# Performance work log

Hardware: AMD Instinct MI355X
Metric: run time of the kernel (lower is better)

The kernel has to match this reference:

```python
import jax, jax.numpy as jnp
import numpy as np

D_MODEL = 2048
N_HEADS = 16
DH = D_MODEL // N_HEADS
B, S, S_CACHE = 2, 1024, 1024


def setup_inputs() -> dict:
    key = jax.random.key(0)
    ks = jax.random.split(key, 5)
    x = jax.random.normal(ks[0], (B, S, D_MODEL), dtype=jnp.float32)
    k_cache = jax.random.normal(ks[1], (B, N_HEADS, S_CACHE, DH), dtype=jnp.float32)
    v_cache = jax.random.normal(ks[2], (B, N_HEADS, S_CACHE, DH), dtype=jnp.float32)
    qkv = 0.01 * jax.random.normal(ks[3], (3 * D_MODEL, D_MODEL), dtype=jnp.float32)
    wo = 0.01 * jax.random.normal(ks[4], (D_MODEL, D_MODEL), dtype=jnp.float32)
    return {"x": x, "k_cache": k_cache, "v_cache": v_cache,
            "qkv": qkv, "wo": wo, "past_length": S_CACHE}


def reference(x, k_cache, v_cache, qkv, wo, past_length):
    Bn, Sn, D = x.shape
    H, dh = N_HEADS, D // N_HEADS
    # Fused QKV projection: (B,S,3D)
    QKV = jnp.einsum('bsd,ed->bse', x, qkv)
    Q, K, V = jnp.split(QKV, 3, axis=-1)
    # (B,H,S,dh)
    q = Q.reshape(Bn, Sn, H, dh).transpose(0, 2, 1, 3)
    k = K.reshape(Bn, Sn, H, dh).transpose(0, 2, 1, 3)
    v = V.reshape(Bn, Sn, H, dh).transpose(0, 2, 1, 3)
    # KV-cache concat along sequence dim
    k_full = jnp.concatenate([k_cache, k], axis=2)
    v_full = jnp.concatenate([v_cache, v], axis=2)
    S_full = k_full.shape[2]
    # Causal mask shifted by past_length: query i attends to keys j <= i + past_length
    rows = jnp.arange(Sn)[:, None]
    cols = jnp.arange(S_full)[None, :]
    allowed = cols <= rows + past_length  # (S, S_full)
    scale = 1.0 / jnp.sqrt(jnp.asarray(dh, x.dtype))
    scores = jnp.einsum('bhqd,bhkd->bhqk', q, k_full) * scale
    scores = jnp.where(allowed[None, None], scores, jnp.finfo(scores.dtype).min)
    attn = jax.nn.softmax(scores, axis=-1)
    ctx = jnp.einsum('bhqk,bhkd->bhqd', attn, v_full)
    out = ctx.transpose(0, 2, 1, 3).reshape(Bn, Sn, D)
    out = jnp.einsum('bsd,ed->bse', out, wo)
    return out, k_full, v_full
```

## Files before the change

### kernel.cpp

```cpp
#include <hip/hip_runtime.h>
#include <cstdint>

#define HB 2
#define HS 1024
#define HSF 2048
#define HH 16
#define HDH 128
#define HD 2048
#define HD3 6144
#define HM 2048

typedef __attribute__((ext_vector_type(8))) short bf16x8;
typedef __attribute__((ext_vector_type(4))) float f32x4;
typedef __attribute__((ext_vector_type(16))) float f32x16;
typedef unsigned short u16;
typedef unsigned int u32;

__device__ __forceinline__ u16 f2b(float f) {
    union { float f; u32 u; } v; v.f = f;
    u32 u = v.u;
    return (u16)((u + 0x7FFFu + ((u >> 16) & 1u)) >> 16);
}
__device__ __forceinline__ float b2f(u16 h) {
    union { u32 u; float f; } v; v.u = ((u32)h) << 16; return v.f;
}

__device__ __forceinline__ f32x4 mfma16x16(bf16x8 a, bf16x8 b, f32x4 c) {
    return __builtin_amdgcn_mfma_f32_16x16x32_bf16(a, b, c, 0, 0, 0);
}
__device__ __forceinline__ f32x16 mfma32x32(bf16x8 a, bf16x8 b, f32x16 c) {
    return __builtin_amdgcn_mfma_f32_32x32x16_bf16(a, b, c, 0, 0, 0);
}
__device__ __forceinline__ void pl32swap(u32 &a, u32 &b) {
    asm volatile("v_permlane32_swap_b32 %0, %1" : "+v"(a), "+v"(b));
}

#define GLD16(gp, lp) __builtin_amdgcn_global_load_lds( \
    (__attribute__((address_space(1))) void*)(gp), \
    (__attribute__((address_space(3))) void*)(lp), 16, 0, 0)

__global__ __launch_bounds__(256) void k_prep(
    const float* __restrict__ x,  u16* __restrict__ xb,  int n0,
    const float* __restrict__ qkv, u16* __restrict__ qkvb, int n1,
    const float* __restrict__ wo,  u16* __restrict__ wob, int n2,
    const float* __restrict__ kc, const float* __restrict__ vc,
    float* __restrict__ kf, float* __restrict__ vf,
    u16* __restrict__ kb, u16* __restrict__ vt)
{
    const int bid = blockIdx.x;
    const int tid = threadIdx.x;
    if (bid < 512) {
        __shared__ u16 Lt[128 * 66];
        int bh = bid >> 4, st = (bid & 15) << 6;
        size_t cbase = (size_t)bh * (HS * HDH) + (size_t)st * HDH;
        size_t fbase = (size_t)bh * (HSF * HDH) + (size_t)st * HDH;
        #pragma unroll
        for (int i = 0; i < 8; ++i) {
            int ci = i * 256 + tid;
            float4 kv = ((const float4*)(kc + cbase))[ci];
            ((float4*)(kf + fbase))[ci] = kv;
            ushort4 k4;
            k4.x = f2b(kv.x); k4.y = f2b(kv.y); k4.z = f2b(kv.z); k4.w = f2b(kv.w);
            ((ushort4*)(kb + fbase))[ci] = k4;
        }
        #pragma unroll
        for (int i = 0; i < 8; ++i) {
            int ci = i * 256 + tid;
            int r = ci >> 5, c = ci & 31;
            float4 vv = ((const float4*)(vc + cbase))[ci];
            ((float4*)(vf + fbase))[ci] = vv;
            int dh = c * 4;
            Lt[(dh + 0) * 66 + r] = f2b(vv.x);
            Lt[(dh + 1) * 66 + r] = f2b(vv.y);
            Lt[(dh + 2) * 66 + r] = f2b(vv.z);
            Lt[(dh + 3) * 66 + r] = f2b(vv.w);
        }
        __syncthreads();
        u16* vtb = vt + (size_t)bh * (HDH * HSF) + st;
        #pragma unroll
        for (int i = 0; i < 4; ++i) {
            int ci = i * 256 + tid;
            int dh = ci >> 3, cs = (ci & 7) * 8;
            const u16* lr = &Lt[dh * 66 + cs];
            ushort4 lo, hi2;
            lo.x = lr[0]; lo.y = lr[1]; lo.z = lr[2]; lo.w = lr[3];
            hi2.x = lr[4]; hi2.y = lr[5]; hi2.z = lr[6]; hi2.w = lr[7];
            u16* dst = vtb + (size_t)dh * HSF + cs;
            *(ushort4*)dst = lo;
            *(ushort4*)(dst + 4) = hi2;
        }
    } else {
        int i = (bid - 512) * 256 + tid;
        const int st_ = ((int)gridDim.x - 512) * 256;
        const int nt = n0 + n1 + n2;
        for (; i < nt; i += st_) {
            const float* s; u16* d; int j = i;
            if (j < n0) { s = x; d = xb; }
            else if (j < n0 + n1) { j -= n0; s = qkv; d = qkvb; }
            else { j -= n0 + n1; s = wo; d = wob; }
            float4 v = ((const float4*)s)[j];
            ushort4 o;
            o.x = f2b(v.x); o.y = f2b(v.y); o.z = f2b(v.z); o.w = f2b(v.w);
            ((ushort4*)d)[j] = o;
        }
    }
}

__global__ __launch_bounds__(256, 2) void k_gemm_qkv(
    const u16* __restrict__ A, const u16* __restrict__ Bw, int K,
    u16* __restrict__ qb, float* __restrict__ kf, float* __restrict__ vf,
    u16* __restrict__ kb, u16* __restrict__ vt)
{
    __shared__ __align__(16) u16 As[2 * 128 * 32];
    __shared__ __align__(16) u16 Bs[2 * 128 * 32];
    const int tid = threadIdx.x;
    const int w = tid >> 6, lane = tid & 63;
    const int wm = w >> 1, wn = w & 1;
    const int lcol = lane & 15, lhi = lane >> 4;

    const int nb = (int)gridDim.x, per = nb >> 3;
    const int bf = (int)blockIdx.x;
    const int t = (bf & 7) * per + (bf >> 3);
    const int m0 = (t & 15) * 128, n0 = (t >> 4) * 128;

    const int srow = lane >> 2;
    const int scol = ((lane & 3) ^ ((lane >> 4) & 2)) * 8;
    const int c0 = w * 2, c1 = w * 2 + 1;
    const u16* Ag0 = A + (size_t)(m0 + c0 * 16 + srow) * K + scol;
    const u16* Ag1 = A + (size_t)(m0 + c1 * 16 + srow) * K + scol;
    const u16* Bg0 = Bw + (size_t)(n0 + c0 * 16 + srow) * K + scol;
    const u16* Bg1 = Bw + (size_t)(n0 + c1 * 16 + srow) * K + scol;

    const int lx = lhi ^ ((lcol >> 2) & 2);

    f32x4 acc[4][4] = {};

    GLD16(Ag0, &As[c0 * 512]);
    GLD16(Ag1, &As[c1 * 512]);
    GLD16(Bg0, &Bs[c0 * 512]);
    GLD16(Bg1, &Bs[c1 * 512]);
    __syncthreads();

    int cur = 0;
    for (int k0 = 0; k0 < K; k0 += 32) {
        if (k0 + 32 < K) {
            int nb_ = (cur ^ 1) * 4096;
            GLD16(Ag0 + k0 + 32, &As[nb_ + c0 * 512]);
            GLD16(Ag1 + k0 + 32, &As[nb_ + c1 * 512]);
            GLD16(Bg0 + k0 + 32, &Bs[nb_ + c0 * 512]);
            GLD16(Bg1 + k0 + 32, &Bs[nb_ + c1 * 512]);
        }
        const int cb = cur * 4096;
        bf16x8 af[4], bfr[4];
        #pragma unroll
        for (int i = 0; i < 4; ++i)
            af[i] = *(const bf16x8*)&As[cb + (wm * 64 + i * 16 + lcol) * 32 + lx * 8];
        #pragma unroll
        for (int i = 0; i < 4; ++i)
            bfr[i] = *(const bf16x8*)&Bs[cb + (wn * 64 + i * 16 + lcol) * 32 + lx * 8];
        __builtin_amdgcn_s_setprio(1);
        #pragma unroll
        for (int i = 0; i < 4; ++i)
            #pragma unroll
            for (int j = 0; j < 4; ++j)
                acc[i][j] = mfma16x16(af[i], bfr[j], acc[i][j]);
        __builtin_amdgcn_s_setprio(0);
        __syncthreads();
        cur ^= 1;
    }

    #pragma unroll
    for (int i = 0; i < 4; ++i) {
      #pragma unroll
      for (int j = 0; j < 4; ++j) {
        #pragma unroll
        for (int r = 0; r < 4; ++r) {
            int m = m0 + wm * 64 + i * 16 + lhi * 4 + r;
            int n = n0 + wn * 64 + j * 16 + lcol;
            float v = acc[i][j][r];
            int b = m >> 10, s = m & 1023;
            int sec = n >> 11, e = n & 2047;
            int h = e >> 7, dh = e & 127;
            int bh = b * HH + h;
            if (sec == 0) {
                qb[((size_t)bh * HS + s) * HDH + dh] = f2b(v * 0.12751742f);
            } else if (sec == 1) {
                size_t idx = ((size_t)bh * HSF + HS + s) * HDH + dh;
                kf[idx] = v; kb[idx] = f2b(v);
            } else {
                size_t idx = ((size_t)bh * HSF + HS + s) * HDH + dh;
                vf[idx] = v;
                vt[((size_t)bh * HDH + dh) * HSF + HS + s] = f2b(v);
            }
        }
      }
    }
}

__global__ __launch_bounds__(256, 4) void k_gemm_out(
    const u16* __restrict__ A, const u16* __restrict__ Bw, int K,
    float* __restrict__ outf)
{
    __shared__ __align__(16) u16 As[2 * 128 * 32];
    __shared__ __align__(16) u16 Bs[2 * 64 * 32];
    const int tid = threadIdx.x;
    const int w = tid >> 6, lane = tid & 63;
    const int wm = w >> 1, wn = w & 1;
    const int lcol = lane & 15, lhi = lane >> 4;

    const int nb = (int)gridDim.x, per = nb >> 3;
    const int bf = (int)blockIdx.x;
    const int t = (bf & 7) * per + (bf >> 3);
    const int m0 = (t & 15) * 128, n0 = (t >> 4) * 64;

    const int srow = lane >> 2;
    const int scol = ((lane & 3) ^ ((lane >> 4) & 2)) * 8;
    const int c0 = w * 2, c1 = w * 2 + 1;
    const u16* Ag0 = A + (size_t)(m0 + c0 * 16 + srow) * K + scol;
    const u16* Ag1 = A + (size_t)(m0 + c1 * 16 + srow) * K + scol;
    const u16* Bg0 = Bw + (size_t)(n0 + w * 16 + srow) * K + scol;

    const int lx = lhi ^ ((lcol >> 2) & 2);

    f32x4 acc[4][2] = {};

    GLD16(Ag0, &As[c0 * 512]);
    GLD16(Ag1, &As[c1 * 512]);
    GLD16(Bg0, &Bs[w * 512]);
    __syncthreads();

    int cur = 0;
    for (int k0 = 0; k0 < K; k0 += 32) {
        if (k0 + 32 < K) {
            GLD16(Ag0 + k0 + 32, &As[(cur ^ 1) * 4096 + c0 * 512]);
            GLD16(Ag1 + k0 + 32, &As[(cur ^ 1) * 4096 + c1 * 512]);
            GLD16(Bg0 + k0 + 32, &Bs[(cur ^ 1) * 2048 + w * 512]);
        }
        const int ca = cur * 4096, cb2 = cur * 2048;
        bf16x8 af[4], bfr[2];
        #pragma unroll
        for (int i = 0; i < 4; ++i)
            af[i] = *(const bf16x8*)&As[ca + (wm * 64 + i * 16 + lcol) * 32 + lx * 8];
        #pragma unroll
        for (int j = 0; j < 2; ++j)
            bfr[j] = *(const bf16x8*)&Bs[cb2 + (wn * 32 + j * 16 + lcol) * 32 + lx * 8];
        __builtin_amdgcn_s_setprio(1);
        #pragma unroll
        for (int i = 0; i < 4; ++i)
            #pragma unroll
            for (int j = 0; j < 2; ++j)
                acc[i][j] = mfma16x16(af[i], bfr[j], acc[i][j]);
        __builtin_amdgcn_s_setprio(0);
        __syncthreads();
        cur ^= 1;
    }

    #pragma unroll
    for (int i = 0; i < 4; ++i)
      #pragma unroll
      for (int j = 0; j < 2; ++j)
        #pragma unroll
        for (int r = 0; r < 4; ++r) {
            int m = m0 + wm * 64 + i * 16 + lhi * 4 + r;
            int n = n0 + wn * 32 + j * 16 + lcol;
            outf[(size_t)m * HD + n] = acc[i][j][r];
        }
}

__global__ __launch_bounds__(256, 3) void k_attn(
    const u16* __restrict__ qb, const u16* __restrict__ kb,
    const u16* __restrict__ vt, u16* __restrict__ pO,
    float* __restrict__ pM, float* __restrict__ pL,
    const int* __restrict__ plp)
{
    __shared__ __align__(16) u16 Ks[64 * 128];
    __shared__ __align__(16) u16 Vs[128 * 64];

    const int past = *plp;
    const int tid = threadIdx.x, w = tid >> 6, lane = tid & 63;
    const int l31 = lane & 31, hi = lane >> 5;

    const int bid = blockIdx.x;
    const int orig = (bid & 7) * 96 + (bid >> 3);
    const int split = orig % 3;
    const int rest = orig / 3;
    const int qblk = rest & 7;
    const int bh = rest >> 3;
    const int q0b = qblk * 128;
    const int q0 = q0b + w * 32;
    const int q = q0 + l31;

    const u16* qx = qb + (size_t)bh * HS * HDH;
    const u16* kx = kb + (size_t)bh * HSF * HDH;
    const u16* vx = vt + (size_t)bh * HDH * HSF;

    bf16x8 qf[8];
    #pragma unroll
    for (int c = 0; c < 8; ++c)
        qf[c] = *(const bf16x8*)&qx[(size_t)q * HDH + c * 16 + hi * 8];

    const int krow0 = w * 16 + (lane >> 4);
    const int kchunk = lane & 15;
    const int vrow0 = w * 32 + (lane >> 3);
    const int vchunk = lane & 7;

    f32x16 o[4] = {};
    float mr = -3e38f, lr = 0.f;

    int nkt = (q0b + 128 + past + 63) >> 6;
    if (nkt > HSF / 64) nkt = HSF / 64;
    const int t0 = (split * nkt) / 3;
    const int t1 = ((split + 1) * nkt) / 3;

    for (int kt = t0; kt < t1; ++kt) {
        const int j0 = kt * 64;
        __syncthreads();
        #pragma unroll
        for (int i = 0; i < 4; ++i) {
            int rk = krow0 + 4 * i;
            GLD16(kx + (size_t)(j0 + rk) * HDH + ((kchunk ^ (rk & 7)) * 8),
                  Ks + w * 2048 + i * 512);
            int rv = vrow0 + 8 * i;
            GLD16(vx + (size_t)rv * HSF + j0 + ((vchunk ^ (rv & 7)) * 8),
                  Vs + w * 2048 + i * 512);
        }
        __syncthreads();

        if (j0 > q0 + 31 + past) continue;

        const char* ksb = (const char*)Ks;
        f32x16 sf0 = {}, sf1 = {};
        const int sw = l31 & 7;
        __builtin_amdgcn_s_setprio(1);
        #pragma unroll
        for (int c = 0; c < 8; ++c) {
            int ch = ((c * 2 + hi) ^ sw) * 16;
            bf16x8 ak0 = *(const bf16x8*)(ksb + l31 * 256 + ch);
            sf0 = mfma32x32(ak0, qf[c], sf0);
            bf16x8 ak1 = *(const bf16x8*)(ksb + (32 + l31) * 256 + ch);
            sf1 = mfma32x32(ak1, qf[c], sf1);
        }
        __builtin_amdgcn_s_setprio(0);

        if (j0 + 63 > q0 + past) {
            #pragma unroll
            for (int r = 0; r < 16; ++r) {
                int ko = (r & 3) + 8 * (r >> 2) + 4 * hi;
                if (j0 + ko > q + past)      sf0[r] = -3e38f;
                if (j0 + 32 + ko > q + past) sf1[r] = -3e38f;
            }
        }
        float pmax = -3e38f;
        #pragma unroll
        for (int r = 0; r < 16; ++r)
            pmax = fmaxf(pmax, fmaxf(sf0[r], sf1[r]));
        pmax = fmaxf(pmax, __shfl_xor(pmax, 32, 64));
        if (!__all((int)(pmax <= mr + 8.f))) {
            float mnew = fmaxf(mr, pmax);
            float alpha = exp2f(mr - mnew);
            mr = mnew;
            lr *= alpha;
            #pragma unroll
            for (int dt = 0; dt < 4; ++dt) o[dt] *= alpha;
        }
        float ps = 0.f;
        #pragma unroll
        for (int r = 0; r < 16; ++r) {
            sf0[r] = exp2f(sf0[r] - mr);
            sf1[r] = exp2f(sf1[r] - mr);
            ps += sf0[r] + sf1[r];
        }
        ps += __shfl_xor(ps, 32, 64);
        lr += ps;

        u32 wA[8], wB[8];
        #pragma unroll
        for (int g = 0; g < 4; ++g) {
            asm("v_cvt_pk_bf16_f32 %0, %1, %2" : "=v"(wA[2*g])   : "v"(sf0[4*g+0]), "v"(sf0[4*g+1]));
            asm("v_cvt_pk_bf16_f32 %0, %1, %2" : "=v"(wA[2*g+1]) : "v"(sf0[4*g+2]), "v"(sf0[4*g+3]));
            asm("v_cvt_pk_bf16_f32 %0, %1, %2" : "=v"(wB[2*g])   : "v"(sf1[4*g+0]), "v"(sf1[4*g+1]));
            asm("v_cvt_pk_bf16_f32 %0, %1, %2" : "=v"(wB[2*g+1]) : "v"(sf1[4*g+2]), "v"(sf1[4*g+3]));
        }
        pl32swap(wA[0], wA[2]); pl32swap(wA[1], wA[3]);
        pl32swap(wA[4], wA[6]); pl32swap(wA[5], wA[7]);
        pl32swap(wB[0], wB[2]); pl32swap(wB[1], wB[3]);
        pl32swap(wB[4], wB[6]); pl32swap(wB[5], wB[7]);
        union uf { u32 u[4]; bf16x8 v; };
        uf pf0, pf1, pf2, pf3;
        pf0.u[0]=wA[0]; pf0.u[1]=wA[1]; pf0.u[2]=wA[2]; pf0.u[3]=wA[3];
        pf1.u[0]=wA[4]; pf1.u[1]=wA[5]; pf1.u[2]=wA[6]; pf1.u[3]=wA[7];
        pf2.u[0]=wB[0]; pf2.u[1]=wB[1]; pf2.u[2]=wB[2]; pf2.u[3]=wB[3];
        pf3.u[0]=wB[4]; pf3.u[1]=wB[5]; pf3.u[2]=wB[6]; pf3.u[3]=wB[7];

        const char* vsb = (const char*)Vs;
        __builtin_amdgcn_s_setprio(1);
        #pragma unroll
        for (int dt = 0; dt < 4; ++dt) {
            int rb = (dt * 32 + l31) * 128;
            bf16x8 av0 = *(const bf16x8*)(vsb + rb + (((0 + hi) ^ sw) * 16));
            o[dt] = mfma32x32(av0, pf0.v, o[dt]);
            bf16x8 av1 = *(const bf16x8*)(vsb + rb + (((2 + hi) ^ sw) * 16));
            o[dt] = mfma32x32(av1, pf1.v, o[dt]);
            bf16x8 av2 = *(const bf16x8*)(vsb + rb + (((4 + hi) ^ sw) * 16));
            o[dt] = mfma32x32(av2, pf2.v, o[dt]);
            bf16x8 av3 = *(const bf16x8*)(vsb + rb + (((6 + hi) ^ sw) * 16));
            o[dt] = mfma32x32(av3, pf3.v, o[dt]);
        }
        __builtin_amdgcn_s_setprio(0);
    }

    const int qg = bh * HS + q;
    if (hi == 0) {
        pM[split * 32768 + qg] = mr;
        pL[split * 32768 + qg] = lr;
    }
    u16* prow = pO + ((size_t)split * 32768 + qg) * 128;
    #pragma unroll
    for (int dt = 0; dt < 4; ++dt)
        #pragma unroll
        for (int g = 0; g < 4; ++g) {
            ushort4 wv;
            wv.x = f2b(o[dt][4*g+0]);
            wv.y = f2b(o[dt][4*g+1]);
            wv.z = f2b(o[dt][4*g+2]);
            wv.w = f2b(o[dt][4*g+3]);
            *(ushort4*)(prow + dt * 32 + 8 * g + 4 * hi) = wv;
        }
}

__global__ __launch_bounds__(256) void k_combine(
    const u16* __restrict__ pO, const float* __restrict__ pM,
    const float* __restrict__ pL, u16* __restrict__ ctx)
{
    int t = blockIdx.x * 256 + threadIdx.x;
    int qg = t >> 5;
    int d4 = (t & 31) << 2;
    float m0 = pM[qg], m1 = pM[32768 + qg], m2 = pM[65536 + qg];
    float l0 = pL[qg], l1 = pL[32768 + qg], l2 = pL[65536 + qg];
    float M = fmaxf(fmaxf(m0, m1), m2);
    float a0 = exp2f(m0 - M), a1 = exp2f(m1 - M), a2 = exp2f(m2 - M);
    float inv = 1.f / (a0 * l0 + a1 * l1 + a2 * l2);
    a0 *= inv; a1 *= inv; a2 *= inv;
    ushort4 v0 = *(const ushort4*)(pO + (size_t)qg * 128 + d4);
    ushort4 v1 = *(const ushort4*)(pO + ((size_t)32768 + qg) * 128 + d4);
    ushort4 v2 = *(const ushort4*)(pO + ((size_t)65536 + qg) * 128 + d4);
    int bh = qg >> 10, qq = qg & 1023;
    int b = bh >> 4, hh = bh & 15;
    u16* crow = ctx + ((size_t)(b * HS + qq)) * HD + hh * HDH + d4;
    ushort4 wv;
    wv.x = f2b(a0 * b2f(v0.x) + a1 * b2f(v1.x) + a2 * b2f(v2.x));
    wv.y = f2b(a0 * b2f(v0.y) + a1 * b2f(v1.y) + a2 * b2f(v2.y));
    wv.z = f2b(a0 * b2f(v0.z) + a1 * b2f(v1.z) + a2 * b2f(v2.z));
    wv.w = f2b(a0 * b2f(v0.w) + a1 * b2f(v1.w) + a2 * b2f(v2.w));
    *(ushort4*)crow = wv;
}

extern "C" void kernel_launch(void* const* d_in, const int* in_sizes, int n_in,
                              void* d_out, int out_size, void* d_ws, size_t ws_size,
                              hipStream_t stream) {
    const float* x   = (const float*)d_in[0];
    const float* kc  = (const float*)d_in[1];
    const float* vc  = (const float*)d_in[2];
    const float* qkv = (const float*)d_in[3];
    const float* wo  = (const float*)d_in[4];
    const int* plp   = (const int*)d_in[5];

    float* out = (float*)d_out;
    float* kf  = out + (size_t)HB * HS * HD;
    float* vf  = kf + (size_t)HB * HH * HSF * HDH;

    char* ws = (char*)d_ws;
    size_t o1 = (size_t)HM * HD * 2;
    size_t o2 = o1 + (size_t)HD3 * HD * 2;
    size_t o3 = o2 + (size_t)HD * HD * 2;
    size_t o4 = o3 + (size_t)HB * HH * HS * HDH * 2;
    size_t o5 = o4 + (size_t)HB * HH * HSF * HDH * 2;
    size_t o6 = o5 + (size_t)HB * HH * HSF * HDH * 2;
    u16* xb   = (u16*)(ws);
    u16* qkvb = (u16*)(ws + o1);
    u16* wob  = (u16*)(ws + o2);
    u16* qb   = (u16*)(ws + o3);
    u16* kb   = (u16*)(ws + o4);
    u16* vt   = (u16*)(ws + o5);
    u16* ctxb = (u16*)(ws + o6);
    u16* pO   = (u16*)ws;
    float* pM = (float*)(ws + (size_t)3 * 32768 * 128 * 2);
    float* pL = (float*)(ws + (size_t)3 * 32768 * 128 * 2 + 393216);

    k_prep<<<2048, 256, 0, stream>>>(x, xb, HM * HD / 4,
                                     qkv, qkvb, HD3 * HD / 4,
                                     wo, wob, HD * HD / 4,
                                     kc, vc, kf, vf, kb, vt);

    k_gemm_qkv<<<768, 256, 0, stream>>>(
        xb, qkvb, HD, qb, kf, vf, kb, vt);

    k_attn<<<768, 256, 0, stream>>>(qb, kb, vt, pO, pM, pL, plp);
    k_combine<<<4096, 256, 0, stream>>>(pO, pM, pL, ctxb);

    k_gemm_out<<<512, 256, 0, stream>>>(ctxb, wob, HD, out);
}
```

Measured before the change: 209.4 us.

## Fuse split-KV combine into attention kernel via last-arriver atomic counter

Removes the separate k_combine launch. Each attention block increments a per-(bh,qblk) counter after writing its partial results, and the third (last) block to arrive merges the three split partials into ctx. Counters are zeroed in the prep kernel. This saves a kernel launch and the gap between the two kernels, but adds a serialized combine tail to some blocks and relies on threadfence and atomic ordering to be correct.

```diff
diff --git a/kernel.cpp b/kernel.cpp
--- a/kernel.cpp
+++ b/kernel.cpp
@@ -45,10 +45,11 @@
     const float* __restrict__ wo,  u16* __restrict__ wob, int n2,
     const float* __restrict__ kc, const float* __restrict__ vc,
     float* __restrict__ kf, float* __restrict__ vf,
-    u16* __restrict__ kb, u16* __restrict__ vt)
+    u16* __restrict__ kb, u16* __restrict__ vt, int* __restrict__ cnt)
 {
     const int bid = blockIdx.x;
     const int tid = threadIdx.x;
+    if (bid == 2047 && tid < 256) cnt[tid] = 0;
     if (bid < 512) {
         __shared__ u16 Lt[128 * 66];
         int bh = bid >> 4, st = (bid & 15) << 6;
@@ -271,10 +272,12 @@
     const u16* __restrict__ qb, const u16* __restrict__ kb,
     const u16* __restrict__ vt, u16* __restrict__ pO,
     float* __restrict__ pM, float* __restrict__ pL,
+    u16* __restrict__ ctx, int* __restrict__ cnt,
     const int* __restrict__ plp)
 {
     __shared__ __align__(16) u16 Ks[64 * 128];
     __shared__ __align__(16) u16 Vs[128 * 64];
+    __shared__ int oldc;
 
     const int past = *plp;
     const int tid = threadIdx.x, w = tid >> 6, lane = tid & 63;
@@ -426,33 +429,36 @@
             wv.w = f2b(o[dt][4*g+3]);
             *(ushort4*)(prow + dt * 32 + 8 * g + 4 * hi) = wv;
         }
-}
-
-__global__ __launch_bounds__(256) void k_combine(
-    const u16* __restrict__ pO, const float* __restrict__ pM,
-    const float* __restrict__ pL, u16* __restrict__ ctx)
-{
-    int t = blockIdx.x * 256 + threadIdx.x;
-    int qg = t >> 5;
-    int d4 = (t & 31) << 2;
-    float m0 = pM[qg], m1 = pM[32768 + qg], m2 = pM[65536 + qg];
-    float l0 = pL[qg], l1 = pL[32768 + qg], l2 = pL[65536 + qg];
-    float M = fmaxf(fmaxf(m0, m1), m2);
-    float a0 = exp2f(m0 - M), a1 = exp2f(m1 - M), a2 = exp2f(m2 - M);
-    float inv = 1.f / (a0 * l0 + a1 * l1 + a2 * l2);
-    a0 *= inv; a1 *= inv; a2 *= inv;
-    ushort4 v0 = *(const ushort4*)(pO + (size_t)qg * 128 + d4);
-    ushort4 v1 = *(const ushort4*)(pO + ((size_t)32768 + qg) * 128 + d4);
-    ushort4 v2 = *(const ushort4*)(pO + ((size_t)65536 + qg) * 128 + d4);
-    int bh = qg >> 10, qq = qg & 1023;
-    int b = bh >> 4, hh = bh & 15;
-    u16* crow = ctx + ((size_t)(b * HS + qq)) * HD + hh * HDH + d4;
-    ushort4 wv;
-    wv.x = f2b(a0 * b2f(v0.x) + a1 * b2f(v1.x) + a2 * b2f(v2.x));
-    wv.y = f2b(a0 * b2f(v0.y) + a1 * b2f(v1.y) + a2 * b2f(v2.y));
-    wv.z = f2b(a0 * b2f(v0.z) + a1 * b2f(v1.z) + a2 * b2f(v2.z));
-    wv.w = f2b(a0 * b2f(v0.w) + a1 * b2f(v1.w) + a2 * b2f(v2.w));
-    *(ushort4*)crow = wv;
+
+    __threadfence();
+    __syncthreads();
+    if (tid == 0) oldc = atomicAdd(&cnt[rest], 1);
+    __syncthreads();
+    if (oldc == 2) {
+        __threadfence();
+        for (int t2 = tid; t2 < 4096; t2 += 256) {
+            int qq = q0b + (t2 >> 5);
+            int qg2 = bh * HS + qq;
+            int d4 = (t2 & 31) << 2;
+            float m0 = pM[qg2], m1 = pM[32768 + qg2], m2 = pM[65536 + qg2];
+            float l0 = pL[qg2], l1 = pL[32768 + qg2], l2 = pL[65536 + qg2];
+            float M = fmaxf(fmaxf(m0, m1), m2);
+            float a0 = exp2f(m0 - M), a1 = exp2f(m1 - M), a2 = exp2f(m2 - M);
+            float inv = 1.f / (a0 * l0 + a1 * l1 + a2 * l2);
+            a0 *= inv; a1 *= inv; a2 *= inv;
+            ushort4 v0 = *(const ushort4*)(pO + (size_t)qg2 * 128 + d4);
+            ushort4 v1 = *(const ushort4*)(pO + ((size_t)32768 + qg2) * 128 + d4);
+            ushort4 v2 = *(const ushort4*)(pO + ((size_t)65536 + qg2) * 128 + d4);
+            int b2 = bh >> 4, hh = bh & 15;
+            u16* crow = ctx + ((size_t)(b2 * HS + qq)) * HD + hh * HDH + d4;
+            ushort4 wv;
+            wv.x = f2b(a0 * b2f(v0.x) + a1 * b2f(v1.x) + a2 * b2f(v2.x));
+            wv.y = f2b(a0 * b2f(v0.y) + a1 * b2f(v1.y) + a2 * b2f(v2.y));
+            wv.z = f2b(a0 * b2f(v0.z) + a1 * b2f(v1.z) + a2 * b2f(v2.z));
+            wv.w = f2b(a0 * b2f(v0.w) + a1 * b2f(v1.w) + a2 * b2f(v2.w));
+            *(ushort4*)crow = wv;
+        }
+    }
 }
 
 extern "C" void kernel_launch(void* const* d_in, const int* in_sizes, int n_in,
@@ -476,6 +482,7 @@
     size_t o4 = o3 + (size_t)HB * HH * HS * HDH * 2;
     size_t o5 = o4 + (size_t)HB * HH * HSF * HDH * 2;
     size_t o6 = o5 + (size_t)HB * HH * HSF * HDH * 2;
+    size_t o7 = o6 + (size_t)HM * HD * 2;
     u16* xb   = (u16*)(ws);
     u16* qkvb = (u16*)(ws + o1);
     u16* wob  = (u16*)(ws + o2);
@@ -483,6 +490,7 @@
     u16* kb   = (u16*)(ws + o4);
     u16* vt   = (u16*)(ws + o5);
     u16* ctxb = (u16*)(ws + o6);
+    int* cnt  = (int*)(ws + o7);
     u16* pO   = (u16*)ws;
     float* pM = (float*)(ws + (size_t)3 * 32768 * 128 * 2);
     float* pL = (float*)(ws + (size_t)3 * 32768 * 128 * 2 + 393216);
@@ -490,13 +498,12 @@
     k_prep<<<2048, 256, 0, stream>>>(x, xb, HM * HD / 4,
                                      qkv, qkvb, HD3 * HD / 4,
                                      wo, wob, HD * HD / 4,
-                                     kc, vc, kf, vf, kb, vt);
+                                     kc, vc, kf, vf, kb, vt, cnt);
 
     k_gemm_qkv<<<768, 256, 0, stream>>>(
         xb, qkvb, HD, qb, kf, vf, kb, vt);
 
-    k_attn<<<768, 256, 0, stream>>>(qb, kb, vt, pO, pM, pL, plp);
-    k_combine<<<4096, 256, 0, stream>>>(pO, pM, pL, ctxb);
+    k_attn<<<768, 256, 0, stream>>>(qb, kb, vt, pO, pM, pL, ctxb, cnt, plp);
 
     k_gemm_out<<<512, 256, 0, stream>>>(ctxb, wob, HD, out);
 }
```

New measurement: 359.7 us. 1.72x slower.
